# Performance work log

Measured on AMD Instinct MI355X. Metric: run time of the kernel, lower is better.

The kernel has to match this reference:

```python
import jax, jax.numpy as jnp
import numpy as np

S, D, H = 2048, 2048, 16
HD = D // H  # head dim = 128
LN_EPS = 1e-5


def _ln(x, g, b):
    mu = jnp.mean(x, axis=-1, keepdims=True)
    var = jnp.var(x, axis=-1, keepdims=True)
    return (x - mu) / jnp.sqrt(var + LN_EPS) * g + b


def setup_inputs() -> dict:
    key = jax.random.key(0)
    ks = jax.random.split(key, 8)
    B = 2
    s = 0.02  # weight init scale
    return {
        "x": jax.random.normal(ks[0], (B, S, D), jnp.float32),
        "Wq": jax.random.normal(ks[1], (D, D), jnp.float32) * s,
        "bq": jnp.zeros((D,), jnp.float32),
        "Wk": jax.random.normal(ks[2], (D, D), jnp.float32) * s,
        "bk": jnp.zeros((D,), jnp.float32),
        "Wv": jax.random.normal(ks[3], (D, D), jnp.float32) * s,
        "bv": jnp.zeros((D,), jnp.float32),
        "Wo": jax.random.normal(ks[4], (D, D), jnp.float32) * s,
        "bo": jnp.zeros((D,), jnp.float32),
        "ln1_g": jnp.ones((D,), jnp.float32),
        "ln1_b": jnp.zeros((D,), jnp.float32),
        "ln2_g": jnp.ones((D,), jnp.float32),
        "ln2_b": jnp.zeros((D,), jnp.float32),
        "W1": jax.random.normal(ks[5], (4 * D, D), jnp.float32) * s,
        "b1": jnp.zeros((4 * D,), jnp.float32),
        "W2": jax.random.normal(ks[6], (D, 4 * D), jnp.float32) * s,
        "b2": jnp.zeros((D,), jnp.float32),
    }


def reference(x, Wq, bq, Wk, bk, Wv, bv, Wo, bo,
              ln1_g, ln1_b, ln2_g, ln2_b, W1, b1, W2, b2):
    causal = jnp.tril(jnp.ones((S, S), bool))  # [S, S] lower-triangular mask
    neg = jnp.finfo(x.dtype).min
    inv_sqrt_hd = 1.0 / jnp.sqrt(jnp.asarray(HD, x.dtype))

    def block(xs):  # xs: [S, D] (equinox module is per-sequence; vmapped over batch)
        h = _ln(xs, ln1_g, ln1_b)
        q = (h @ Wq.T + bq).reshape(S, H, HD)
        k = (h @ Wk.T + bk).reshape(S, H, HD)
        v = (h @ Wv.T + bv).reshape(S, H, HD)
        logits = jnp.einsum('shd,Shd->hsS', q, k) * inv_sqrt_hd
        logits = jnp.where(causal, logits, neg)
        attn = jax.nn.softmax(logits, axis=-1)
        o = jnp.einsum('hsS,Shd->shd', attn, v).reshape(S, D)
        h = h + (o @ Wo.T + bo)          # residual of post-ln1 value (as in source)
        h2 = _ln(h, ln2_g, ln2_b)
        m = jax.nn.gelu(h2 @ W1.T + b1) @ W2.T + b2
        return h2 + m                    # residual of post-ln2 value (as in source)

    return jax.vmap(block)(x)
```

## Files before the change

### kernel.cpp

```cpp
#include <hip/hip_runtime.h>
#include <hip/hip_bf16.h>
#include <math.h>

#define DD   2048
#define SS   2048
#define HH   16
#define HDIM 128
#define BB   2
#define MM   4096
#define D4   8192

using bf16x8 = __attribute__((ext_vector_type(8))) short;
using f32x4  = __attribute__((ext_vector_type(4))) float;
using f32x16 = __attribute__((ext_vector_type(16))) float;

__device__ __forceinline__ ushort f2bf(float x) {
  uint u = __builtin_bit_cast(uint, x);
  u += 0x7FFFu + ((u >> 16) & 1u);
  return (ushort)(u >> 16);
}
__device__ __forceinline__ float bf2f(ushort u) {
  return __builtin_bit_cast(float, (uint)u << 16);
}
__device__ __forceinline__ uint pkbf2(float a, float b) {
  return (uint)f2bf(a) | ((uint)f2bf(b) << 16);
}

__device__ __forceinline__ float gelu_f(float v) {
  float u = 0.7978845608028654f * (v + 0.044715f * v * v * v);
  float e = __expf(2.0f * u);
  float th = 1.0f - 2.0f / (e + 1.0f);
  return 0.5f * v * (1.0f + th);
}

__device__ __forceinline__ void gload_lds16(const void* g, void* l) {
  __builtin_amdgcn_global_load_lds(
      (const __attribute__((address_space(1))) void*)g,
      (__attribute__((address_space(3))) void*)l, 16, 0, 0);
}

__global__ __launch_bounds__(256) void cvt_f32_bf16(
    const float* __restrict__ in, ushort* __restrict__ out, int n4) {
  int i = blockIdx.x * 256 + threadIdx.x;
  if (i >= n4) return;
  float4 v = ((const float4*)in)[i];
  ushort4 o;
  o.x = f2bf(v.x); o.y = f2bf(v.y); o.z = f2bf(v.z); o.w = f2bf(v.w);
  ((ushort4*)out)[i] = o;
}

__global__ __launch_bounds__(256) void ln_rows(
    const float* __restrict__ in, const float* __restrict__ gam,
    const float* __restrict__ bet, ushort* __restrict__ outb) {
  int row = blockIdx.x;
  int t = threadIdx.x;
  const float4* r4 = (const float4*)(in + (size_t)row * DD);
  float4 v0 = r4[t], v1 = r4[t + 256];
  float s = v0.x + v0.y + v0.z + v0.w + v1.x + v1.y + v1.z + v1.w;
  __shared__ float redA[4], redB[4];
  #pragma unroll
  for (int off = 32; off >= 1; off >>= 1) s += __shfl_xor(s, off);
  if ((t & 63) == 0) redA[t >> 6] = s;
  __syncthreads();
  float mean = (redA[0] + redA[1] + redA[2] + redA[3]) * (1.0f / DD);
  float d0 = v0.x - mean, d1 = v0.y - mean, d2 = v0.z - mean, d3 = v0.w - mean;
  float d4 = v1.x - mean, d5 = v1.y - mean, d6 = v1.z - mean, d7 = v1.w - mean;
  float q = d0*d0 + d1*d1 + d2*d2 + d3*d3 + d4*d4 + d5*d5 + d6*d6 + d7*d7;
  #pragma unroll
  for (int off = 32; off >= 1; off >>= 1) q += __shfl_xor(q, off);
  if ((t & 63) == 0) redB[t >> 6] = q;
  __syncthreads();
  float var = (redB[0] + redB[1] + redB[2] + redB[3]) * (1.0f / DD);
  float rstd = rsqrtf(var + 1e-5f);
  const float4* g4 = (const float4*)gam;
  const float4* b4 = (const float4*)bet;
  float4 g0 = g4[t], g1 = g4[t + 256], bb0 = b4[t], bb1 = b4[t + 256];
  float4 y0, y1;
  y0.x = d0 * rstd * g0.x + bb0.x;  y0.y = d1 * rstd * g0.y + bb0.y;
  y0.z = d2 * rstd * g0.z + bb0.z;  y0.w = d3 * rstd * g0.w + bb0.w;
  y1.x = d4 * rstd * g1.x + bb1.x;  y1.y = d5 * rstd * g1.y + bb1.y;
  y1.z = d6 * rstd * g1.z + bb1.z;  y1.w = d7 * rstd * g1.w + bb1.w;
  ushort4 u0, u1;
  u0.x = f2bf(y0.x); u0.y = f2bf(y0.y); u0.z = f2bf(y0.z); u0.w = f2bf(y0.w);
  u1.x = f2bf(y1.x); u1.y = f2bf(y1.y); u1.z = f2bf(y1.z); u1.w = f2bf(y1.w);
  ushort4* ob4 = (ushort4*)(outb + (size_t)row * DD);
  ob4[t] = u0; ob4[t + 256] = u1;
}

template <int OMODE, bool GELU_, bool RES_>
__global__ __launch_bounds__(512, 2) void gemm2(
    const ushort* __restrict__ A, const ushort* __restrict__ Bt,
    const float* __restrict__ pb0, const ushort* __restrict__ res,
    void* __restrict__ Cout, int M, int N, int K) {
  extern __shared__ __align__(16) ushort smem[];
  const int nbm = M >> 8, nbn = N >> 7;
  const int nwg = nbm * nbn;
  int wg = blockIdx.x;
  int wg2 = (wg & 7) * (nwg >> 3) + (wg >> 3);
  int bm = wg2 % nbm, bn = wg2 / nbm;
  int m0 = bm << 8, n0 = bn << 7;
  int t = threadIdx.x, lane = t & 63, w = t >> 6;
  int wm = w >> 2, wn = w & 3;
  int lr = lane & 15, lg = lane >> 4;

  auto stage = [&](int kt, int slot) {
    int k0 = kt << 6;
    ushort* lA = smem + slot * 24576;
    ushort* lB = lA + 16384;
    #pragma unroll
    for (int r = 0; r < 4; r++) {
      int idx = (r << 9) + t;
      int row = idx >> 3, ch = idx & 7;
      gload_lds16(A + (size_t)(m0 + row) * K + k0 + ((ch ^ (row & 7)) << 3),
                  lA + idx * 8);
    }
    #pragma unroll
    for (int r = 0; r < 2; r++) {
      int idx = (r << 9) + t;
      int row = idx >> 3, ch = idx & 7;
      gload_lds16(Bt + (size_t)(n0 + row) * K + k0 + ((ch ^ (row & 7)) << 3),
                  lB + idx * 8);
    }
  };

  f32x4 acc[8][2] = {};
  const int NT = K >> 6;
  stage(0, 0);
  stage(1, 1);
  int slot = 0;
  for (int kt = 0; kt < NT; ++kt) {
    __builtin_amdgcn_sched_barrier(0);
    if (kt + 1 < NT)
      asm volatile("s_waitcnt vmcnt(6) lgkmcnt(0)" ::: "memory");
    else
      asm volatile("s_waitcnt vmcnt(0) lgkmcnt(0)" ::: "memory");
    __builtin_amdgcn_s_barrier();
    __builtin_amdgcn_sched_barrier(0);
    if (kt + 2 < NT) {
      int s2 = slot + 2; if (s2 >= 3) s2 -= 3;
      stage(kt + 2, s2);
    }
    const ushort* lA = smem + slot * 24576;
    const ushort* lB = lA + 16384;
    bf16x8 af[8][2], bfr[2][2];
    #pragma unroll
    for (int mi = 0; mi < 8; mi++) {
      int row = wm * 128 + mi * 16 + lr;
      #pragma unroll
      for (int ks = 0; ks < 2; ks++)
        af[mi][ks] = *(const bf16x8*)
            &lA[row * 64 + (((ks * 4 + lg) ^ (row & 7)) << 3)];
    }
    #pragma unroll
    for (int ni = 0; ni < 2; ni++) {
      int row = wn * 32 + ni * 16 + lr;
      #pragma unroll
      for (int ks = 0; ks < 2; ks++)
        bfr[ni][ks] = *(const bf16x8*)
            &lB[row * 64 + (((ks * 4 + lg) ^ (row & 7)) << 3)];
    }
    __builtin_amdgcn_s_setprio(1);
    #pragma unroll
    for (int ks = 0; ks < 2; ks++)
      #pragma unroll
      for (int mi = 0; mi < 8; mi++)
        #pragma unroll
        for (int ni = 0; ni < 2; ni++)
          acc[mi][ni] = __builtin_amdgcn_mfma_f32_16x16x32_bf16(
              af[mi][ks], bfr[ni][ks], acc[mi][ni], 0, 0, 0);
    __builtin_amdgcn_s_setprio(0);
    slot = (slot + 1 == 3) ? 0 : slot + 1;
  }

  float bv[2];
  #pragma unroll
  for (int ni = 0; ni < 2; ni++) bv[ni] = pb0[n0 + wn * 32 + ni * 16 + lr];
  #pragma unroll
  for (int mi = 0; mi < 8; mi++) {
    #pragma unroll
    for (int r = 0; r < 4; r++) {
      int m = m0 + wm * 128 + mi * 16 + lg * 4 + r;
      #pragma unroll
      for (int ni = 0; ni < 2; ni++) {
        int n = n0 + wn * 32 + ni * 16 + lr;
        size_t idx = (size_t)m * N + n;
        float v = acc[mi][ni][r] + bv[ni];
        if (RES_) v += bf2f(res[idx]);
        if (GELU_) v = gelu_f(v);
        if (OMODE == 1) ((ushort*)Cout)[idx] = f2bf(v);
        else            ((float*)Cout)[idx] = v;
      }
    }
  }
}

#define MF16(MQ, NQ, BARR) \
  { _Pragma("unroll") for (int ks = 0; ks < 2; ks++) { \
    _Pragma("unroll") for (int fm = 0; fm < 4; fm++) { \
      _Pragma("unroll") for (int fn = 0; fn < 2; fn++) { \
        acc[MQ * 4 + fm][NQ * 2 + fn] = \
            __builtin_amdgcn_mfma_f32_16x16x32_bf16( \
                aR[fm][ks], BARR[fn][ks], acc[MQ * 4 + fm][NQ * 2 + fn], \
                0, 0, 0); } } } }

template <int OMODE, bool GELU_>
__global__ __launch_bounds__(512, 2) void gemm8(
    const ushort* __restrict__ A, const ushort* __restrict__ Bt,
    const float* __restrict__ pb0, const float* __restrict__ pb1,
    const float* __restrict__ pb2,
    void* __restrict__ Cout, int M, int N, int Kfull, int Kloc) {
  extern __shared__ __align__(16) ushort smem[];
  const int nbm = M >> 8, nbn = N >> 8;
  const int nwg = nbm * nbn;
  int wgr = blockIdx.x;
  int ksl = 0;
  if (OMODE == 4) { ksl = wgr / nwg; wgr -= ksl * nwg; }
  int wg2 = (wgr & 7) * (nwg >> 3) + (wgr >> 3);
  int bm = wg2 % nbm, bn = wg2 / nbm;
  int m0 = bm << 8, n0 = bn << 8;
  size_t kbase = (size_t)ksl * Kloc;
  int t = threadIdx.x, lane = t & 63, w = t >> 6;
  int wm = w >> 2, wn = w & 3;
  int lr = lane & 15, lg = lane >> 4;

  int srow = t >> 3;
  int ssw = ((t & 7) ^ (srow & 7)) << 3;
  const ushort* pA1 = A + (size_t)(m0 + srow) * Kfull + kbase + ssw;
  const ushort* pB1 = Bt +
      (size_t)(n0 + (srow >> 5) * 64 + (srow & 31)) * Kfull + kbase + ssw;
  const size_t K32 = (size_t)32 * Kfull, K64 = (size_t)64 * Kfull,
               K128 = (size_t)128 * Kfull;
  ushort* dA = smem + t * 8;
  ushort* dB = smem + 16384 + t * 8;

  auto stage = [&](int kt, int h) {
    int boff = (kt & 1) << 15;
    size_t ko = (size_t)kt << 6;
    if (h < 2) {
      const ushort* g = pA1 + (size_t)h * K64 + ko;
      ushort* d = dA + boff + h * 8192;
      gload_lds16(g, d);
      gload_lds16(g + K128, d + 4096);
    } else {
      const ushort* g = pB1 + (size_t)(h - 2) * K32 + ko;
      ushort* d = dB + boff + (h - 2) * 8192;
      gload_lds16(g, d);
      gload_lds16(g + K128, d + 4096);
    }
  };

  int swz0 = (lg ^ (lr & 7)) << 3;
  int swz1 = ((4 + lg) ^ (lr & 7)) << 3;
  int arb[4], brb[2];
  #pragma unroll
  for (int f = 0; f < 4; f++) arb[f] = (wm * 64 + f * 16 + lr) * 64;
  #pragma unroll
  for (int f = 0; f < 2; f++) brb[f] = (wn * 32 + f * 16 + lr) * 64;

  f32x4 acc[8][4] = {};
  bf16x8 aR[4][2], bR0[2][2], bR1[2][2];
  const int NT = Kloc >> 6;

  stage(0, 0); stage(0, 1); stage(0, 2); stage(0, 3);
  asm volatile("s_waitcnt vmcnt(0)" ::: "memory");
  __builtin_amdgcn_s_barrier();

  for (int kt = 0; kt < NT; ++kt) {
    const ushort* hA = smem + ((kt & 1) << 15);
    const ushort* hB = hA + 16384;
    bool st = (kt + 1 < NT);
    #pragma unroll
    for (int f = 0; f < 4; f++) {
      aR[f][0] = *(const bf16x8*)&hA[arb[f] + swz0];
      aR[f][1] = *(const bf16x8*)&hA[arb[f] + swz1];
    }
    #pragma unroll
    for (int f = 0; f < 2; f++) {
      bR0[f][0] = *(const bf16x8*)&hB[brb[f] + swz0];
      bR0[f][1] = *(const bf16x8*)&hB[brb[f] + swz1];
    }
    if (st) stage(kt + 1, 0);
    asm volatile("s_waitcnt lgkmcnt(8)" ::: "memory");
    __builtin_amdgcn_sched_barrier(0);
    __builtin_amdgcn_s_barrier();
    asm volatile("s_waitcnt lgkmcnt(0)" ::: "memory");
    __builtin_amdgcn_sched_barrier(0);
    __builtin_amdgcn_s_setprio(1);
    MF16(0, 0, bR0);
    __builtin_amdgcn_s_setprio(0);
    __builtin_amdgcn_sched_barrier(0);
    if (st) { asm volatile("s_waitcnt vmcnt(4)" ::: "memory"); }
    else    { asm volatile("s_waitcnt vmcnt(2)" ::: "memory"); }
    __builtin_amdgcn_s_barrier();
    #pragma unroll
    for (int f = 0; f < 2; f++) {
      bR1[f][0] = *(const bf16x8*)&hB[8192 + brb[f] + swz0];
      bR1[f][1] = *(const bf16x8*)&hB[8192 + brb[f] + swz1];
    }
    if (st) stage(kt + 1, 2);
    __builtin_amdgcn_sched_barrier(0);
    __builtin_amdgcn_s_barrier();
    asm volatile("s_waitcnt lgkmcnt(0)" ::: "memory");
    __builtin_amdgcn_sched_barrier(0);
    __builtin_amdgcn_s_setprio(1);
    MF16(0, 1, bR1);
    __builtin_amdgcn_s_setprio(0);
    __builtin_amdgcn_sched_barrier(0);
    if (st) { asm volatile("s_waitcnt vmcnt(4)" ::: "memory"); }
    else    { asm volatile("s_waitcnt vmcnt(0)" ::: "memory"); }
    __builtin_amdgcn_s_barrier();
    #pragma unroll
    for (int f = 0; f < 4; f++) {
      aR[f][0] = *(const bf16x8*)&hA[8192 + arb[f] + swz0];
      aR[f][1] = *(const bf16x8*)&hA[8192 + arb[f] + swz1];
    }
    if (st) stage(kt + 1, 3);
    __builtin_amdgcn_sched_barrier(0);
    __builtin_amdgcn_s_barrier();
    asm volatile("s_waitcnt lgkmcnt(0)" ::: "memory");
    __builtin_amdgcn_sched_barrier(0);
    __builtin_amdgcn_s_setprio(1);
    MF16(1, 1, bR1);
    __builtin_amdgcn_s_setprio(0);
    __builtin_amdgcn_sched_barrier(0);
    __builtin_amdgcn_s_barrier();
    if (st) stage(kt + 1, 1);
    __builtin_amdgcn_sched_barrier(0);
    __builtin_amdgcn_s_barrier();
    __builtin_amdgcn_sched_barrier(0);
    __builtin_amdgcn_s_setprio(1);
    MF16(1, 0, bR0);
    __builtin_amdgcn_s_setprio(0);
    __builtin_amdgcn_sched_barrier(0);
    if (st) { asm volatile("s_waitcnt vmcnt(4)" ::: "memory"); }
    __builtin_amdgcn_s_barrier();
  }

  if constexpr (OMODE == 4) {
    ushort* Cp = (ushort*)Cout + (size_t)ksl * M * N;
    #pragma unroll
    for (int mi = 0; mi < 8; mi++) {
      #pragma unroll
      for (int r = 0; r < 4; r++) {
        int m = m0 + wm * 128 + mi * 16 + lg * 4 + r;
        #pragma unroll
        for (int ni = 0; ni < 4; ni++) {
          int n = n0 + wn * 64 + ni * 16 + lr;
          Cp[(size_t)m * N + n] = f2bf(acc[mi][ni][r]);
        }
      }
    }
  } else if constexpr (OMODE == 3) {
    int seg = n0 >> 11;
    const float* pb = (seg == 0) ? pb0 : (seg == 1) ? pb1 : pb2;
    int c0 = n0 & 2047;
    float bv[4];
    #pragma unroll
    for (int ni = 0; ni < 4; ni++) bv[ni] = pb[c0 + wn * 64 + ni * 16 + lr];
    if (seg < 2) {
      ushort* q_or_k = (ushort*)Cout + (size_t)seg * MM * DD;
      #pragma unroll
      for (int mi = 0; mi < 8; mi++) {
        #pragma unroll
        for (int r = 0; r < 4; r++) {
          int m = m0 + wm * 128 + mi * 16 + lg * 4 + r;
          #pragma unroll
          for (int ni = 0; ni < 4; ni++) {
            int col = c0 + wn * 64 + ni * 16 + lr;
            q_or_k[(size_t)m * DD + col] = f2bf(acc[mi][ni][r] + bv[ni]);
          }
        }
      }
    } else {
      ushort* vT = (ushort*)Cout + (size_t)2 * MM * DD;
      #pragma unroll
      for (int mi = 0; mi < 8; mi++) {
        int mg = m0 + wm * 128 + mi * 16 + lg * 4;
        int bb_ = mg >> 11, sb = mg & 2047;
        #pragma unroll
        for (int ni = 0; ni < 4; ni++) {
          int col = c0 + wn * 64 + ni * 16 + lr;
          int h = col >> 7, d = col & 127;
          ushort4 u4;
          u4.x = f2bf(acc[mi][ni][0] + bv[ni]);
          u4.y = f2bf(acc[mi][ni][1] + bv[ni]);
          u4.z = f2bf(acc[mi][ni][2] + bv[ni]);
          u4.w = f2bf(acc[mi][ni][3] + bv[ni]);
          size_t idx = ((size_t)(bb_ * 16 + h) * 128 + d) * 2048 + sb;
          *(ushort4*)&vT[idx] = u4;
        }
      }
    }
  } else {
    float bv[4];
    #pragma unroll
    for (int ni = 0; ni < 4; ni++) bv[ni] = pb0[n0 + wn * 64 + ni * 16 + lr];
    #pragma unroll
    for (int mi = 0; mi < 8; mi++) {
      #pragma unroll
      for (int r = 0; r < 4; r++) {
        int m = m0 + wm * 128 + mi * 16 + lg * 4 + r;
        #pragma unroll
        for (int ni = 0; ni < 4; ni++) {
          int n = n0 + wn * 64 + ni * 16 + lr;
          float v = acc[mi][ni][r] + bv[ni];
          if (GELU_) v = gelu_f(v);
          ((ushort*)Cout)[(size_t)m * N + n] = f2bf(v);
        }
      }
    }
  }
}

__global__ __launch_bounds__(256) void mlp_fin(
    const ushort* __restrict__ p, const ushort* __restrict__ res,
    const float* __restrict__ bias, float* __restrict__ out) {
  int i4 = blockIdx.x * 256 + threadIdx.x;
  ushort4 a = ((const ushort4*)p)[i4];
  ushort4 b = ((const ushort4*)(p + (size_t)MM * DD))[i4];
  ushort4 r = ((const ushort4*)res)[i4];
  float4 g = ((const float4*)bias)[i4 & 511];
  float4 o;
  o.x = bf2f(a.x) + bf2f(b.x) + bf2f(r.x) + g.x;
  o.y = bf2f(a.y) + bf2f(b.y) + bf2f(r.y) + g.y;
  o.z = bf2f(a.z) + bf2f(b.z) + bf2f(r.z) + g.z;
  o.w = bf2f(a.w) + bf2f(b.w) + bf2f(r.w) + g.w;
  ((float4*)out)[i4] = o;
}

__global__ __launch_bounds__(256) void attn_fwd(
    const ushort* __restrict__ qb, const ushort* __restrict__ kb,
    const ushort* __restrict__ vTb, ushort* __restrict__ ob) {
  extern __shared__ __align__(16) ushort asm_[];
  ushort* KsB = asm_;
  ushort* VsB = asm_ + 16384;
  ushort* Pw  = asm_ + 32768 + (threadIdx.x >> 6) * 2048;

  int blk = blockIdx.x;
  int i15 = blk & 15;
  int qt = (blk & 256) ? i15 : 15 - i15;
  int bh = blk >> 4;
  int b = bh >> 4, h = bh & 15;
  int q0 = qt << 7;
  int t = threadIdx.x, lane = t & 63, w = t >> 6;
  int l31 = lane & 31, hi = lane >> 5;
  const size_t base = (size_t)b * SS * DD + (size_t)h * HDIM;
  const ushort* qp = qb + base;
  const ushort* kp = kb + base;
  const ushort* vp = vTb + (size_t)bh * HDIM * SS;
  int wq0 = q0 + w * 32;
  int qg = wq0 + l31;

  bf16x8 qf[8];
  #pragma unroll
  for (int kk = 0; kk < 8; kk++)
    qf[kk] = *(const bf16x8*)(qp + (size_t)qg * DD + kk * 16 + hi * 8);

  auto stageKV = [&](int it, int buf) {
    int kv0 = it * 64;
    ushort* Kd = KsB + buf * 8192;
    ushort* Vd = VsB + buf * 8192;
    #pragma unroll
    for (int ii = 0; ii < 4; ii++) {
      int chunk = ii * 256 + t;
      int row = chunk >> 4, cc = chunk & 15;
      gload_lds16(kp + (size_t)(kv0 + row) * DD + ((cc ^ (row & 15)) << 3),
                  Kd + chunk * 8);
    }
    #pragma unroll
    for (int ii = 0; ii < 4; ii++) {
      int chunk = ii * 256 + t;
      int row = chunk >> 3, cc = chunk & 7;
      gload_lds16(vp + (size_t)row * SS + kv0 + ((cc ^ (row & 7)) << 3),
                  Vd + chunk * 8);
    }
  };

  f32x16 o[4] = {};
  float mu = -1e30f, lrow = 0.f;
  const float csc = 0.08838834764831845f * 1.4426950408889634f;

  int nIter = 2 * qt + 2;
  stageKV(0, 0);
  asm volatile("s_waitcnt vmcnt(0)" ::: "memory");
  __builtin_amdgcn_s_barrier();
  int cur = 0;
  for (int it = 0; it < nIter; ++it) {
    int kv0 = it * 64;
    if (it + 1 < nIter) stageKV(it + 1, cur ^ 1);

    if (kv0 <= wq0 + 31) {
      const ushort* Kc = KsB + cur * 8192;
      const ushort* Vc = VsB + cur * 8192;
      f32x16 s2[2] = {};
      #pragma unroll
      for (int nt = 0; nt < 2; nt++) {
        int row = nt * 32 + l31;
        #pragma unroll
        for (int kk = 0; kk < 8; kk++) {
          bf16x8 kf = *(const bf16x8*)
              &Kc[row * 128 + (((kk * 2 + hi) ^ (row & 15)) << 3)];
          s2[nt] = __builtin_amdgcn_mfma_f32_32x32x16_bf16(kf, qf[kk], s2[nt],
                                                           0, 0, 0);
        }
      }
      bool full = (kv0 + 63 <= wq0);
      float pm[4] = {-3e38f, -3e38f, -3e38f, -3e38f};
      if (full) {
        #pragma unroll
        for (int nt = 0; nt < 2; nt++)
          #pragma unroll
          for (int g2 = 0; g2 < 4; g2++)
            #pragma unroll
            for (int i = 0; i < 4; i++) {
              float u = s2[nt][g2 * 4 + i] * csc;
              s2[nt][g2 * 4 + i] = u;
              pm[i] = fmaxf(pm[i], u);
            }
      } else {
        #pragma unroll
        for (int nt = 0; nt < 2; nt++)
          #pragma unroll
          for (int g2 = 0; g2 < 4; g2++)
            #pragma unroll
            for (int i = 0; i < 4; i++) {
              int kvl = nt * 32 + g2 * 8 + 4 * hi + i;
              float u = (kv0 + kvl > qg) ? -3e38f : s2[nt][g2 * 4 + i] * csc;
              s2[nt][g2 * 4 + i] = u;
              pm[i] = fmaxf(pm[i], u);
            }
      }
      float mx = fmaxf(fmaxf(pm[0], pm[1]), fmaxf(pm[2], pm[3]));
      mx = fmaxf(mx, __shfl_xor(mx, 32));
      if (!__all(mx - mu <= 8.0f)) {
        float mnew = fmaxf(mu, mx);
        float fr = exp2f(mu - mnew);
        mu = mnew;
        lrow *= fr;
        #pragma unroll
        for (int dt = 0; dt < 4; dt++)
          #pragma unroll
          for (int r = 0; r < 16; r++) o[dt][r] *= fr;
      }
      float ps[4] = {0.f, 0.f, 0.f, 0.f};
      #pragma unroll
      for (int nt = 0; nt < 2; nt++)
        #pragma unroll
        for (int g2 = 0; g2 < 4; g2++)
          #pragma unroll
          for (int i = 0; i < 4; i++) {
            float p = exp2f(s2[nt][g2 * 4 + i] - mu);
            s2[nt][g2 * 4 + i] = p;
            ps[i] += p;
          }
      float sum = (ps[0] + ps[1]) + (ps[2] + ps[3]);
      sum += __shfl_xor(sum, 32);
      lrow += sum;
      #pragma unroll
      for (int nt = 0; nt < 2; nt++) {
        #pragma unroll
        for (int g2 = 0; g2 < 4; g2++) {
          uint2 u;
          u.x = pkbf2(s2[nt][g2 * 4 + 0], s2[nt][g2 * 4 + 1]);
          u.y = pkbf2(s2[nt][g2 * 4 + 2], s2[nt][g2 * 4 + 3]);
          int cp = (nt * 4 + g2) ^ (l31 & 7);
          *(uint2*)&Pw[l31 * 64 + cp * 8 + hi * 4] = u;
        }
      }
      asm volatile("s_waitcnt lgkmcnt(0)" ::: "memory");
      #pragma unroll
      for (int kk = 0; kk < 4; kk++) {
        bf16x8 pf = *(const bf16x8*)
            &Pw[l31 * 64 + (((kk * 2 + hi) ^ (l31 & 7)) << 3)];
        #pragma unroll
        for (int dt = 0; dt < 4; dt++) {
          int drow = dt * 32 + l31;
          bf16x8 vf = *(const bf16x8*)
              &Vc[drow * 64 + (((kk * 2 + hi) ^ (drow & 7)) << 3)];
          o[dt] = __builtin_amdgcn_mfma_f32_32x32x16_bf16(vf, pf, o[dt],
                                                          0, 0, 0);
        }
      }
    }
    asm volatile("s_waitcnt vmcnt(0)" ::: "memory");
    __builtin_amdgcn_s_barrier();
    cur ^= 1;
  }

  float inv = 1.0f / lrow;
  #pragma unroll
  for (int dt = 0; dt < 4; dt++) {
    #pragma unroll
    for (int g2 = 0; g2 < 4; g2++) {
      uint2 u;
      u.x = pkbf2(o[dt][g2 * 4 + 0] * inv, o[dt][g2 * 4 + 1] * inv);
      u.y = pkbf2(o[dt][g2 * 4 + 2] * inv, o[dt][g2 * 4 + 3] * inv);
      int d = dt * 32 + 8 * g2 + 4 * hi;
      *(uint2*)&ob[base + (size_t)qg * DD + d] = u;
    }
  }
}

extern "C" void kernel_launch(void* const* d_in, const int* in_sizes, int n_in,
                              void* d_out, int out_size, void* d_ws,
                              size_t ws_size, hipStream_t stream) {
  const float* x    = (const float*)d_in[0];
  const float* Wq   = (const float*)d_in[1];
  const float* bq   = (const float*)d_in[2];
  const float* Wk   = (const float*)d_in[3];
  const float* bk   = (const float*)d_in[4];
  const float* Wv   = (const float*)d_in[5];
  const float* bv   = (const float*)d_in[6];
  const float* Wo   = (const float*)d_in[7];
  const float* bo   = (const float*)d_in[8];
  const float* ln1g = (const float*)d_in[9];
  const float* ln1b = (const float*)d_in[10];
  const float* ln2g = (const float*)d_in[11];
  const float* ln2b = (const float*)d_in[12];
  const float* W1   = (const float*)d_in[13];
  const float* b1   = (const float*)d_in[14];
  const float* W2   = (const float*)d_in[15];
  const float* b2   = (const float*)d_in[16];

  char* ws = (char*)d_ws;
  ushort* Wqkvb = (ushort*)(ws);
  ushort* Wob   = Wqkvb + (size_t)3 * DD * DD;
  ushort* W1b = (ushort*)(ws);
  ushort* W2b = W1b + (size_t)D4 * DD;
  ushort* qkvb = (ushort*)(ws + 67108864);
  ushort* qbf = qkvb;
  ushort* kbf = qbf + (size_t)MM * DD;
  ushort* vTt = kbf + (size_t)MM * DD;
  ushort* aob = vTt + (size_t)MM * DD;
  ushort* gb  = (ushort*)(ws + 67108864);
  ushort* hb  = (ushort*)(ws + 167772160);
  ushort* h2b = hb;
  float* h2in = (float*)(ws + 184549376);
  ushort* pD  = (ushort*)(ws + 184549376);
  float* out  = (float*)d_out;

  const int LDSB = 147456;
  const int LDSC = 131072;
  const int LDSA = 81920;
  (void)hipFuncSetAttribute((const void*)gemm2<0, false, true>,
                      hipFuncAttributeMaxDynamicSharedMemorySize, LDSB);
  (void)hipFuncSetAttribute((const void*)gemm8<3, false>,
                      hipFuncAttributeMaxDynamicSharedMemorySize, LDSC);
  (void)hipFuncSetAttribute((const void*)gemm8<1, true>,
                      hipFuncAttributeMaxDynamicSharedMemorySize, LDSC);
  (void)hipFuncSetAttribute((const void*)gemm8<4, false>,
                      hipFuncAttributeMaxDynamicSharedMemorySize, LDSC);
  (void)hipFuncSetAttribute((const void*)attn_fwd,
                      hipFuncAttributeMaxDynamicSharedMemorySize, LDSA);

  dim3 blk(256);
  dim3 gblk(512);
  cvt_f32_bf16<<<DD * DD / 1024, blk, 0, stream>>>(Wq, Wqkvb, DD * DD / 4);
  cvt_f32_bf16<<<DD * DD / 1024, blk, 0, stream>>>(Wk, Wqkvb + (size_t)DD * DD, DD * DD / 4);
  cvt_f32_bf16<<<DD * DD / 1024, blk, 0, stream>>>(Wv, Wqkvb + (size_t)2 * DD * DD, DD * DD / 4);
  cvt_f32_bf16<<<DD * DD / 1024, blk, 0, stream>>>(Wo, Wob, DD * DD / 4);
  ln_rows<<<MM, blk, 0, stream>>>(x, ln1g, ln1b, hb);
  gemm8<3, false><<<384, gblk, LDSC, stream>>>(
      hb, Wqkvb, bq, bk, bv, qkvb, MM, 3 * DD, DD, DD);
  attn_fwd<<<512, blk, LDSA, stream>>>(qbf, kbf, vTt, aob);
  gemm2<0, false, true><<<256, gblk, LDSB, stream>>>(
      aob, Wob, bo, hb, h2in, MM, DD, DD);
  ln_rows<<<MM, blk, 0, stream>>>(h2in, ln2g, ln2b, h2b);
  cvt_f32_bf16<<<D4 * DD / 1024, blk, 0, stream>>>(W1, W1b, D4 * DD / 4);
  cvt_f32_bf16<<<D4 * DD / 1024, blk, 0, stream>>>(W2, W2b, D4 * DD / 4);
  gemm8<1, true><<<512, gblk, LDSC, stream>>>(
      h2b, W1b, b1, b1, b1, gb, MM, D4, DD, DD);
  gemm8<4, false><<<256, gblk, LDSC, stream>>>(
      gb, W2b, b2, b2, b2, pD, MM, DD, D4, D4 / 2);
  mlp_fin<<<MM * DD / 1024, blk, 0, stream>>>(pD, h2b, b2, out);
}
```

Before: 637.9 us.

## Move QKV and W2 projections to 256x128 gemm2, drop split-K and mlp_fin

The QKV projection moves from the 256x256-tile gemm8 (384 workgroups) to the 256x128-tile gemm2 kernel (768 workgroups), whose epilogue now writes Q and K plus the transposed V. The W2 down-projection drops its split-K=2 gemm8 pass and the separate mlp_fin reduction kernel, and instead uses gemm2 with a fused bias and residual epilogue writing fp32 output directly. This removes the bf16 partial-sum round trip and one kernel launch, and raises workgroup counts for better occupancy, at the cost of smaller tiles with less operand reuse and a long K=8192 loop across only 256 workgroups for W2.

```diff
diff --git a/kernel.cpp b/kernel.cpp
--- a/kernel.cpp
+++ b/kernel.cpp
@@ -90,7 +90,8 @@
 template <int OMODE, bool GELU_, bool RES_>
 __global__ __launch_bounds__(512, 2) void gemm2(
     const ushort* __restrict__ A, const ushort* __restrict__ Bt,
-    const float* __restrict__ pb0, const ushort* __restrict__ res,
+    const float* __restrict__ pb0, const float* __restrict__ pb1,
+    const float* __restrict__ pb2, const ushort* __restrict__ res,
     void* __restrict__ Cout, int M, int N, int K) {
   extern __shared__ __align__(16) ushort smem[];
   const int nbm = M >> 8, nbn = N >> 7;
@@ -172,6 +173,50 @@
     slot = (slot + 1 == 3) ? 0 : slot + 1;
   }
 
+  if (OMODE == 3) {
+    int seg = n0 >> 11;
+    const float* pb = (seg == 0) ? pb0 : (seg == 1) ? pb1 : pb2;
+    int c0 = n0 & 2047;
+    float bv[2];
+    #pragma unroll
+    for (int ni = 0; ni < 2; ni++) bv[ni] = pb[c0 + wn * 32 + ni * 16 + lr];
+    if (seg < 2) {
+      ushort* q_or_k = (ushort*)Cout + (size_t)seg * MM * DD;
+      #pragma unroll
+      for (int mi = 0; mi < 8; mi++) {
+        #pragma unroll
+        for (int r = 0; r < 4; r++) {
+          int m = m0 + wm * 128 + mi * 16 + lg * 4 + r;
+          #pragma unroll
+          for (int ni = 0; ni < 2; ni++) {
+            int col = c0 + wn * 32 + ni * 16 + lr;
+            q_or_k[(size_t)m * DD + col] = f2bf(acc[mi][ni][r] + bv[ni]);
+          }
+        }
+      }
+    } else {
+      ushort* vT = (ushort*)Cout + (size_t)2 * MM * DD;
+      #pragma unroll
+      for (int mi = 0; mi < 8; mi++) {
+        int mg = m0 + wm * 128 + mi * 16 + lg * 4;
+        int bb_ = mg >> 11, sb = mg & 2047;
+        #pragma unroll
+        for (int ni = 0; ni < 2; ni++) {
+          int col = c0 + wn * 32 + ni * 16 + lr;
+          int h = col >> 7, d = col & 127;
+          ushort4 u4;
+          u4.x = f2bf(acc[mi][ni][0] + bv[ni]);
+          u4.y = f2bf(acc[mi][ni][1] + bv[ni]);
+          u4.z = f2bf(acc[mi][ni][2] + bv[ni]);
+          u4.w = f2bf(acc[mi][ni][3] + bv[ni]);
+          size_t idx = ((size_t)(bb_ * 16 + h) * 128 + d) * 2048 + sb;
+          *(ushort4*)&vT[idx] = u4;
+        }
+      }
+    }
+    return;
+  }
+
   float bv[2];
   #pragma unroll
   for (int ni = 0; ni < 2; ni++) bv[ni] = pb0[n0 + wn * 32 + ni * 16 + lr];
@@ -206,28 +251,24 @@
 template <int OMODE, bool GELU_>
 __global__ __launch_bounds__(512, 2) void gemm8(
     const ushort* __restrict__ A, const ushort* __restrict__ Bt,
-    const float* __restrict__ pb0, const float* __restrict__ pb1,
-    const float* __restrict__ pb2,
-    void* __restrict__ Cout, int M, int N, int Kfull, int Kloc) {
+    const float* __restrict__ pb0,
+    void* __restrict__ Cout, int M, int N, int Kfull) {
   extern __shared__ __align__(16) ushort smem[];
   const int nbm = M >> 8, nbn = N >> 8;
   const int nwg = nbm * nbn;
   int wgr = blockIdx.x;
-  int ksl = 0;
-  if (OMODE == 4) { ksl = wgr / nwg; wgr -= ksl * nwg; }
   int wg2 = (wgr & 7) * (nwg >> 3) + (wgr >> 3);
   int bm = wg2 % nbm, bn = wg2 / nbm;
   int m0 = bm << 8, n0 = bn << 8;
-  size_t kbase = (size_t)ksl * Kloc;
   int t = threadIdx.x, lane = t & 63, w = t >> 6;
   int wm = w >> 2, wn = w & 3;
   int lr = lane & 15, lg = lane >> 4;
 
   int srow = t >> 3;
   int ssw = ((t & 7) ^ (srow & 7)) << 3;
-  const ushort* pA1 = A + (size_t)(m0 + srow) * Kfull + kbase + ssw;
+  const ushort* pA1 = A + (size_t)(m0 + srow) * Kfull + ssw;
   const ushort* pB1 = Bt +
-      (size_t)(n0 + (srow >> 5) * 64 + (srow & 31)) * Kfull + kbase + ssw;
+      (size_t)(n0 + (srow >> 5) * 64 + (srow & 31)) * Kfull + ssw;
   const size_t K32 = (size_t)32 * Kfull, K64 = (size_t)64 * Kfull,
                K128 = (size_t)128 * Kfull;
   ushort* dA = smem + t * 8;
@@ -259,7 +300,7 @@
 
   f32x4 acc[8][4] = {};
   bf16x8 aR[4][2], bR0[2][2], bR1[2][2];
-  const int NT = Kloc >> 6;
+  const int NT = Kfull >> 6;
 
   stage(0, 0); stage(0, 1); stage(0, 2); stage(0, 3);
   asm volatile("s_waitcnt vmcnt(0)" ::: "memory");
@@ -336,96 +377,23 @@
     __builtin_amdgcn_s_barrier();
   }
 
-  if constexpr (OMODE == 4) {
-    ushort* Cp = (ushort*)Cout + (size_t)ksl * M * N;
-    #pragma unroll
-    for (int mi = 0; mi < 8; mi++) {
-      #pragma unroll
-      for (int r = 0; r < 4; r++) {
-        int m = m0 + wm * 128 + mi * 16 + lg * 4 + r;
-        #pragma unroll
-        for (int ni = 0; ni < 4; ni++) {
-          int n = n0 + wn * 64 + ni * 16 + lr;
-          Cp[(size_t)m * N + n] = f2bf(acc[mi][ni][r]);
-        }
-      }
-    }
-  } else if constexpr (OMODE == 3) {
-    int seg = n0 >> 11;
-    const float* pb = (seg == 0) ? pb0 : (seg == 1) ? pb1 : pb2;
-    int c0 = n0 & 2047;
-    float bv[4];
-    #pragma unroll
-    for (int ni = 0; ni < 4; ni++) bv[ni] = pb[c0 + wn * 64 + ni * 16 + lr];
-    if (seg < 2) {
-      ushort* q_or_k = (ushort*)Cout + (size_t)seg * MM * DD;
-      #pragma unroll
-      for (int mi = 0; mi < 8; mi++) {
-        #pragma unroll
-        for (int r = 0; r < 4; r++) {
-          int m = m0 + wm * 128 + mi * 16 + lg * 4 + r;
-          #pragma unroll
-          for (int ni = 0; ni < 4; ni++) {
-            int col = c0 + wn * 64 + ni * 16 + lr;
-            q_or_k[(size_t)m * DD + col] = f2bf(acc[mi][ni][r] + bv[ni]);
-          }
-        }
-      }
-    } else {
-      ushort* vT = (ushort*)Cout + (size_t)2 * MM * DD;
-      #pragma unroll
-      for (int mi = 0; mi < 8; mi++) {
-        int mg = m0 + wm * 128 + mi * 16 + lg * 4;
-        int bb_ = mg >> 11, sb = mg & 2047;
-        #pragma unroll
-        for (int ni = 0; ni < 4; ni++) {
-          int col = c0 + wn * 64 + ni * 16 + lr;
-          int h = col >> 7, d = col & 127;
-          ushort4 u4;
-          u4.x = f2bf(acc[mi][ni][0] + bv[ni]);
-          u4.y = f2bf(acc[mi][ni][1] + bv[ni]);
-          u4.z = f2bf(acc[mi][ni][2] + bv[ni]);
-          u4.w = f2bf(acc[mi][ni][3] + bv[ni]);
-          size_t idx = ((size_t)(bb_ * 16 + h) * 128 + d) * 2048 + sb;
-          *(ushort4*)&vT[idx] = u4;
-        }
-      }
-    }
-  } else {
-    float bv[4];
-    #pragma unroll
-    for (int ni = 0; ni < 4; ni++) bv[ni] = pb0[n0 + wn * 64 + ni * 16 + lr];
-    #pragma unroll
-    for (int mi = 0; mi < 8; mi++) {
-      #pragma unroll
-      for (int r = 0; r < 4; r++) {
-        int m = m0 + wm * 128 + mi * 16 + lg * 4 + r;
-        #pragma unroll
-        for (int ni = 0; ni < 4; ni++) {
-          int n = n0 + wn * 64 + ni * 16 + lr;
-          float v = acc[mi][ni][r] + bv[ni];
-          if (GELU_) v = gelu_f(v);
-          ((ushort*)Cout)[(size_t)m * N + n] = f2bf(v);
-        }
+  float bv[4];
+  #pragma unroll
+  for (int ni = 0; ni < 4; ni++) bv[ni] = pb0[n0 + wn * 64 + ni * 16 + lr];
+  #pragma unroll
+  for (int mi = 0; mi < 8; mi++) {
+    #pragma unroll
+    for (int r = 0; r < 4; r++) {
+      int m = m0 + wm * 128 + mi * 16 + lg * 4 + r;
+      #pragma unroll
+      for (int ni = 0; ni < 4; ni++) {
+        int n = n0 + wn * 64 + ni * 16 + lr;
+        float v = acc[mi][ni][r] + bv[ni];
+        if (GELU_) v = gelu_f(v);
+        ((ushort*)Cout)[(size_t)m * N + n] = f2bf(v);
       }
     }
   }
-}
-
-__global__ __launch_bounds__(256) void mlp_fin(
-    const ushort* __restrict__ p, const ushort* __restrict__ res,
-    const float* __restrict__ bias, float* __restrict__ out) {
-  int i4 = blockIdx.x * 256 + threadIdx.x;
-  ushort4 a = ((const ushort4*)p)[i4];
-  ushort4 b = ((const ushort4*)(p + (size_t)MM * DD))[i4];
-  ushort4 r = ((const ushort4*)res)[i4];
-  float4 g = ((const float4*)bias)[i4 & 511];
-  float4 o;
-  o.x = bf2f(a.x) + bf2f(b.x) + bf2f(r.x) + g.x;
-  o.y = bf2f(a.y) + bf2f(b.y) + bf2f(r.y) + g.y;
-  o.z = bf2f(a.z) + bf2f(b.z) + bf2f(r.z) + g.z;
-  o.w = bf2f(a.w) + bf2f(b.w) + bf2f(r.w) + g.w;
-  ((float4*)out)[i4] = o;
 }
 
 __global__ __launch_bounds__(256) void attn_fwd(
@@ -636,19 +604,16 @@
   ushort* hb  = (ushort*)(ws + 167772160);
   ushort* h2b = hb;
   float* h2in = (float*)(ws + 184549376);
-  ushort* pD  = (ushort*)(ws + 184549376);
   float* out  = (float*)d_out;
 
   const int LDSB = 147456;
   const int LDSC = 131072;
   const int LDSA = 81920;
+  (void)hipFuncSetAttribute((const void*)gemm2<3, false, false>,
+                      hipFuncAttributeMaxDynamicSharedMemorySize, LDSB);
   (void)hipFuncSetAttribute((const void*)gemm2<0, false, true>,
                       hipFuncAttributeMaxDynamicSharedMemorySize, LDSB);
-  (void)hipFuncSetAttribute((const void*)gemm8<3, false>,
-                      hipFuncAttributeMaxDynamicSharedMemorySize, LDSC);
   (void)hipFuncSetAttribute((const void*)gemm8<1, true>,
-                      hipFuncAttributeMaxDynamicSharedMemorySize, LDSC);
-  (void)hipFuncSetAttribute((const void*)gemm8<4, false>,
                       hipFuncAttributeMaxDynamicSharedMemorySize, LDSC);
   (void)hipFuncSetAttribute((const void*)attn_fwd,
                       hipFuncAttributeMaxDynamicSharedMemorySize, LDSA);
@@ -660,17 +625,16 @@
   cvt_f32_bf16<<<DD * DD / 1024, blk, 0, stream>>>(Wv, Wqkvb + (size_t)2 * DD * DD, DD * DD / 4);
   cvt_f32_bf16<<<DD * DD / 1024, blk, 0, stream>>>(Wo, Wob, DD * DD / 4);
   ln_rows<<<MM, blk, 0, stream>>>(x, ln1g, ln1b, hb);
-  gemm8<3, false><<<384, gblk, LDSC, stream>>>(
-      hb, Wqkvb, bq, bk, bv, qkvb, MM, 3 * DD, DD, DD);
+  gemm2<3, false, false><<<768, gblk, LDSB, stream>>>(
+      hb, Wqkvb, bq, bk, bv, nullptr, qkvb, MM, 3 * DD, DD);
   attn_fwd<<<512, blk, LDSA, stream>>>(qbf, kbf, vTt, aob);
   gemm2<0, false, true><<<256, gblk, LDSB, stream>>>(
-      aob, Wob, bo, hb, h2in, MM, DD, DD);
+      aob, Wob, bo, bo, bo, hb, h2in, MM, DD, DD);
   ln_rows<<<MM, blk, 0, stream>>>(h2in, ln2g, ln2b, h2b);
   cvt_f32_bf16<<<D4 * DD / 1024, blk, 0, stream>>>(W1, W1b, D4 * DD / 4);
   cvt_f32_bf16<<<D4 * DD / 1024, blk, 0, stream>>>(W2, W2b, D4 * DD / 4);
   gemm8<1, true><<<512, gblk, LDSC, stream>>>(
-      h2b, W1b, b1, b1, b1, gb, MM, D4, DD, DD);
-  gemm8<4, false><<<256, gblk, LDSC, stream>>>(
-      gb, W2b, b2, b2, b2, pD, MM, DD, D4, D4 / 2);
-  mlp_fin<<<MM * DD / 1024, blk, 0, stream>>>(pD, h2b, b2, out);
-}
+      h2b, W1b, b1, gb, MM, D4, DD);
+  gemm2<0, false, true><<<256, gblk, LDSB, stream>>>(
+      gb, W2b, b2, b2, b2, h2b, out, MM, DD, D4);
+}
```

Measured after the change: 616.6 us. -3.3%, faster.

## Deepen gemm8 prefetch to two k-tiles ahead and move QKV GEMM to gemm2

Applied to the files above, without the earlier changes.

The main-loop staging in gemm8 now issues global-to-LDS loads for tile kt+2 instead of kt+1. Two tiles are preloaded in the prologue, and the vmcnt waits move to once per iteration. The goal is to hide more memory latency in the large MLP GEMMs. The QKV projection moves to the 256x128-tile gemm2 kernel with 768 workgroups, carrying over the q/k/vT split epilogue, to improve CU fill over the earlier 384 large tiles. The risks are LDS write-after-read hazards, since the next-but-one tile is written into the buffer currently being read, and a heavier store epilogue with half-width tiles.

```diff
diff --git a/kernel.cpp b/kernel.cpp
--- a/kernel.cpp
+++ b/kernel.cpp
@@ -90,7 +90,8 @@
 template <int OMODE, bool GELU_, bool RES_>
 __global__ __launch_bounds__(512, 2) void gemm2(
     const ushort* __restrict__ A, const ushort* __restrict__ Bt,
-    const float* __restrict__ pb0, const ushort* __restrict__ res,
+    const float* __restrict__ pb0, const float* __restrict__ pb1,
+    const float* __restrict__ pb2, const ushort* __restrict__ res,
     void* __restrict__ Cout, int M, int N, int K) {
   extern __shared__ __align__(16) ushort smem[];
   const int nbm = M >> 8, nbn = N >> 7;
@@ -172,6 +173,50 @@
     slot = (slot + 1 == 3) ? 0 : slot + 1;
   }
 
+  if (OMODE == 3) {
+    int seg = n0 >> 11;
+    const float* pb = (seg == 0) ? pb0 : (seg == 1) ? pb1 : pb2;
+    int c0 = n0 & 2047;
+    float bv[2];
+    #pragma unroll
+    for (int ni = 0; ni < 2; ni++) bv[ni] = pb[c0 + wn * 32 + ni * 16 + lr];
+    if (seg < 2) {
+      ushort* q_or_k = (ushort*)Cout + (size_t)seg * MM * DD;
+      #pragma unroll
+      for (int mi = 0; mi < 8; mi++) {
+        #pragma unroll
+        for (int r = 0; r < 4; r++) {
+          int m = m0 + wm * 128 + mi * 16 + lg * 4 + r;
+          #pragma unroll
+          for (int ni = 0; ni < 2; ni++) {
+            int col = c0 + wn * 32 + ni * 16 + lr;
+            q_or_k[(size_t)m * DD + col] = f2bf(acc[mi][ni][r] + bv[ni]);
+          }
+        }
+      }
+    } else {
+      ushort* vT = (ushort*)Cout + (size_t)2 * MM * DD;
+      #pragma unroll
+      for (int mi = 0; mi < 8; mi++) {
+        int mg = m0 + wm * 128 + mi * 16 + lg * 4;
+        int bb_ = mg >> 11, sb = mg & 2047;
+        #pragma unroll
+        for (int ni = 0; ni < 2; ni++) {
+          int col = c0 + wn * 32 + ni * 16 + lr;
+          int h = col >> 7, d = col & 127;
+          ushort4 u4;
+          u4.x = f2bf(acc[mi][ni][0] + bv[ni]);
+          u4.y = f2bf(acc[mi][ni][1] + bv[ni]);
+          u4.z = f2bf(acc[mi][ni][2] + bv[ni]);
+          u4.w = f2bf(acc[mi][ni][3] + bv[ni]);
+          size_t idx = ((size_t)(bb_ * 16 + h) * 128 + d) * 2048 + sb;
+          *(ushort4*)&vT[idx] = u4;
+        }
+      }
+    }
+    return;
+  }
+
   float bv[2];
   #pragma unroll
   for (int ni = 0; ni < 2; ni++) bv[ni] = pb0[n0 + wn * 32 + ni * 16 + lr];
@@ -206,8 +251,7 @@
 template <int OMODE, bool GELU_>
 __global__ __launch_bounds__(512, 2) void gemm8(
     const ushort* __restrict__ A, const ushort* __restrict__ Bt,
-    const float* __restrict__ pb0, const float* __restrict__ pb1,
-    const float* __restrict__ pb2,
+    const float* __restrict__ pb0,
     void* __restrict__ Cout, int M, int N, int Kfull, int Kloc) {
   extern __shared__ __align__(16) ushort smem[];
   const int nbm = M >> 8, nbn = N >> 8;
@@ -262,13 +306,14 @@
   const int NT = Kloc >> 6;
 
   stage(0, 0); stage(0, 1); stage(0, 2); stage(0, 3);
-  asm volatile("s_waitcnt vmcnt(0)" ::: "memory");
+  stage(1, 0); stage(1, 1); stage(1, 2); stage(1, 3);
+  asm volatile("s_waitcnt vmcnt(8)" ::: "memory");
   __builtin_amdgcn_s_barrier();
 
   for (int kt = 0; kt < NT; ++kt) {
     const ushort* hA = smem + ((kt & 1) << 15);
     const ushort* hB = hA + 16384;
-    bool st = (kt + 1 < NT);
+    bool st2 = (kt + 2 < NT);
     #pragma unroll
     for (int f = 0; f < 4; f++) {
       aR[f][0] = *(const bf16x8*)&hA[arb[f] + swz0];
@@ -279,7 +324,6 @@
       bR0[f][0] = *(const bf16x8*)&hB[brb[f] + swz0];
       bR0[f][1] = *(const bf16x8*)&hB[brb[f] + swz1];
     }
-    if (st) stage(kt + 1, 0);
     asm volatile("s_waitcnt lgkmcnt(8)" ::: "memory");
     __builtin_amdgcn_sched_barrier(0);
     __builtin_amdgcn_s_barrier();
@@ -289,15 +333,13 @@
     MF16(0, 0, bR0);
     __builtin_amdgcn_s_setprio(0);
     __builtin_amdgcn_sched_barrier(0);
-    if (st) { asm volatile("s_waitcnt vmcnt(4)" ::: "memory"); }
-    else    { asm volatile("s_waitcnt vmcnt(2)" ::: "memory"); }
     __builtin_amdgcn_s_barrier();
     #pragma unroll
     for (int f = 0; f < 2; f++) {
       bR1[f][0] = *(const bf16x8*)&hB[8192 + brb[f] + swz0];
       bR1[f][1] = *(const bf16x8*)&hB[8192 + brb[f] + swz1];
     }
-    if (st) stage(kt + 1, 2);
+    if (st2) { stage(kt + 2, 0); stage(kt + 2, 2); }
     __builtin_amdgcn_sched_barrier(0);
     __builtin_amdgcn_s_barrier();
     asm volatile("s_waitcnt lgkmcnt(0)" ::: "memory");
@@ -306,15 +348,13 @@
     MF16(0, 1, bR1);
     __builtin_amdgcn_s_setprio(0);
     __builtin_amdgcn_sched_barrier(0);
-    if (st) { asm volatile("s_waitcnt vmcnt(4)" ::: "memory"); }
-    else    { asm volatile("s_waitcnt vmcnt(0)" ::: "memory"); }
     __builtin_amdgcn_s_barrier();
     #pragma unroll
     for (int f = 0; f < 4; f++) {
       aR[f][0] = *(const bf16x8*)&hA[8192 + arb[f] + swz0];
       aR[f][1] = *(const bf16x8*)&hA[8192 + arb[f] + swz1];
     }
-    if (st) stage(kt + 1, 3);
+    if (st2) stage(kt + 2, 3);
     __builtin_amdgcn_sched_barrier(0);
     __builtin_amdgcn_s_barrier();
     asm volatile("s_waitcnt lgkmcnt(0)" ::: "memory");
@@ -324,7 +364,7 @@
     __builtin_amdgcn_s_setprio(0);
     __builtin_amdgcn_sched_barrier(0);
     __builtin_amdgcn_s_barrier();
-    if (st) stage(kt + 1, 1);
+    if (st2) stage(kt + 2, 1);
     __builtin_amdgcn_sched_barrier(0);
     __builtin_amdgcn_s_barrier();
     __builtin_amdgcn_sched_barrier(0);
@@ -332,7 +372,8 @@
     MF16(1, 0, bR0);
     __builtin_amdgcn_s_setprio(0);
     __builtin_amdgcn_sched_barrier(0);
-    if (st) { asm volatile("s_waitcnt vmcnt(4)" ::: "memory"); }
+    if (st2)              { asm volatile("s_waitcnt vmcnt(8)" ::: "memory"); }
+    else if (kt + 1 < NT) { asm volatile("s_waitcnt vmcnt(0)" ::: "memory"); }
     __builtin_amdgcn_s_barrier();
   }
 
@@ -347,47 +388,6 @@
         for (int ni = 0; ni < 4; ni++) {
           int n = n0 + wn * 64 + ni * 16 + lr;
           Cp[(size_t)m * N + n] = f2bf(acc[mi][ni][r]);
-        }
-      }
-    }
-  } else if constexpr (OMODE == 3) {
-    int seg = n0 >> 11;
-    const float* pb = (seg == 0) ? pb0 : (seg == 1) ? pb1 : pb2;
-    int c0 = n0 & 2047;
-    float bv[4];
-    #pragma unroll
-    for (int ni = 0; ni < 4; ni++) bv[ni] = pb[c0 + wn * 64 + ni * 16 + lr];
-    if (seg < 2) {
-      ushort* q_or_k = (ushort*)Cout + (size_t)seg * MM * DD;
-      #pragma unroll
-      for (int mi = 0; mi < 8; mi++) {
-        #pragma unroll
-        for (int r = 0; r < 4; r++) {
-          int m = m0 + wm * 128 + mi * 16 + lg * 4 + r;
-          #pragma unroll
-          for (int ni = 0; ni < 4; ni++) {
-            int col = c0 + wn * 64 + ni * 16 + lr;
-            q_or_k[(size_t)m * DD + col] = f2bf(acc[mi][ni][r] + bv[ni]);
-          }
-        }
-      }
-    } else {
-      ushort* vT = (ushort*)Cout + (size_t)2 * MM * DD;
-      #pragma unroll
-      for (int mi = 0; mi < 8; mi++) {
-        int mg = m0 + wm * 128 + mi * 16 + lg * 4;
-        int bb_ = mg >> 11, sb = mg & 2047;
-        #pragma unroll
-        for (int ni = 0; ni < 4; ni++) {
-          int col = c0 + wn * 64 + ni * 16 + lr;
-          int h = col >> 7, d = col & 127;
-          ushort4 u4;
-          u4.x = f2bf(acc[mi][ni][0] + bv[ni]);
-          u4.y = f2bf(acc[mi][ni][1] + bv[ni]);
-          u4.z = f2bf(acc[mi][ni][2] + bv[ni]);
-          u4.w = f2bf(acc[mi][ni][3] + bv[ni]);
-          size_t idx = ((size_t)(bb_ * 16 + h) * 128 + d) * 2048 + sb;
-          *(ushort4*)&vT[idx] = u4;
         }
       }
     }
@@ -642,10 +642,10 @@
   const int LDSB = 147456;
   const int LDSC = 131072;
   const int LDSA = 81920;
+  (void)hipFuncSetAttribute((const void*)gemm2<3, false, false>,
+                      hipFuncAttributeMaxDynamicSharedMemorySize, LDSB);
   (void)hipFuncSetAttribute((const void*)gemm2<0, false, true>,
                       hipFuncAttributeMaxDynamicSharedMemorySize, LDSB);
-  (void)hipFuncSetAttribute((const void*)gemm8<3, false>,
-                      hipFuncAttributeMaxDynamicSharedMemorySize, LDSC);
   (void)hipFuncSetAttribute((const void*)gemm8<1, true>,
                       hipFuncAttributeMaxDynamicSharedMemorySize, LDSC);
   (void)hipFuncSetAttribute((const void*)gemm8<4, false>,
@@ -660,17 +660,17 @@
   cvt_f32_bf16<<<DD * DD / 1024, blk, 0, stream>>>(Wv, Wqkvb + (size_t)2 * DD * DD, DD * DD / 4);
   cvt_f32_bf16<<<DD * DD / 1024, blk, 0, stream>>>(Wo, Wob, DD * DD / 4);
   ln_rows<<<MM, blk, 0, stream>>>(x, ln1g, ln1b, hb);
-  gemm8<3, false><<<384, gblk, LDSC, stream>>>(
-      hb, Wqkvb, bq, bk, bv, qkvb, MM, 3 * DD, DD, DD);
+  gemm2<3, false, false><<<768, gblk, LDSB, stream>>>(
+      hb, Wqkvb, bq, bk, bv, nullptr, qkvb, MM, 3 * DD, DD);
   attn_fwd<<<512, blk, LDSA, stream>>>(qbf, kbf, vTt, aob);
   gemm2<0, false, true><<<256, gblk, LDSB, stream>>>(
-      aob, Wob, bo, hb, h2in, MM, DD, DD);
+      aob, Wob, bo, bo, bo, hb, h2in, MM, DD, DD);
   ln_rows<<<MM, blk, 0, stream>>>(h2in, ln2g, ln2b, h2b);
   cvt_f32_bf16<<<D4 * DD / 1024, blk, 0, stream>>>(W1, W1b, D4 * DD / 4);
   cvt_f32_bf16<<<D4 * DD / 1024, blk, 0, stream>>>(W2, W2b, D4 * DD / 4);
   gemm8<1, true><<<512, gblk, LDSC, stream>>>(
-      h2b, W1b, b1, b1, b1, gb, MM, D4, DD, DD);
+      h2b, W1b, b1, gb, MM, D4, DD, DD);
   gemm8<4, false><<<256, gblk, LDSC, stream>>>(
-      gb, W2b, b2, b2, b2, pD, MM, DD, D4, D4 / 2);
+      gb, W2b, b2, pD, MM, DD, D4, D4 / 2);
   mlp_fin<<<MM * DD / 1024, blk, 0, stream>>>(pD, h2b, b2, out);
 }
```

Measured after the change: 620.7 us. -2.7%, faster.
